# Kernel optimization log

Measured on AMD Instinct MI355X. Metric: run time of the kernel, lower is better.

## Reference

```python
import jax, jax.numpy as jnp
import numpy as np

OOV_INDEX = 1  # stand-in for params.OOV_INDEX
H = 1024
VOCAB = 50000
L = 2048


def setup_inputs() -> dict:
    key = jax.random.key(0)
    ks = jax.random.split(key, 10)
    s = 0.05
    inp = {
        "input_ids": jax.random.randint(ks[0], (L,), 0, VOCAB),
        "embedding": jax.random.normal(ks[1], (VOCAB, H), jnp.float32) * s,
        "fwd_W_ih": jax.random.normal(ks[2], (3 * H, H), jnp.float32) * s,
        "fwd_W_hh": jax.random.normal(ks[3], (3 * H, H), jnp.float32) * s,
        "fwd_b_ih": jax.random.normal(ks[4], (3 * H,), jnp.float32) * s,
        "fwd_b_hh": jax.random.normal(ks[5], (3 * H,), jnp.float32) * s,
        "rev_W_ih": jax.random.normal(ks[6], (3 * H, H), jnp.float32) * s,
        "rev_W_hh": jax.random.normal(ks[7], (3 * H, H), jnp.float32) * s,
        "rev_b_ih": jax.random.normal(ks[8], (3 * H,), jnp.float32) * s,
        "rev_b_hh": jax.random.normal(ks[9], (3 * H,), jnp.float32) * s,
    }
    return inp


def _gru_scan(x_seq, W_ih, W_hh, b_ih, b_hh):
    # x_seq: [L, H]. PyTorch GRU gate order: r, z, n.
    gx = x_seq @ W_ih.T + b_ih  # [L, 3H], input projections precomputed

    def step(h, gx_t):
        gh = h @ W_hh.T + b_hh
        gx_r, gx_z, gx_n = jnp.split(gx_t, 3)
        gh_r, gh_z, gh_n = jnp.split(gh, 3)
        r = jax.nn.sigmoid(gx_r + gh_r)
        z = jax.nn.sigmoid(gx_z + gh_z)
        n = jnp.tanh(gx_n + r * gh_n)
        h_new = (1.0 - z) * n + z * h
        return h_new, h_new

    h0 = jnp.zeros((x_seq.shape[1],), x_seq.dtype)
    h_last, outs = jax.lax.scan(step, h0, gx)
    return outs, h_last  # [L, H], [H]


def reference(input_ids, embedding, fwd_W_ih, fwd_W_hh, fwd_b_ih, fwd_b_hh,
              rev_W_ih, rev_W_hh, rev_b_ih, rev_b_hh):
    # Embedding lookup; OOV index -> zero vector (empty_vector in original)
    embeds = embedding[input_ids]  # [L, H]
    embeds = jnp.where((input_ids == OOV_INDEX)[:, None], 0.0, embeds)

    fwd_outputs, fwd_h = _gru_scan(embeds, fwd_W_ih, fwd_W_hh, fwd_b_ih, fwd_b_hh)
    rev_outs_rev, rev_h = _gru_scan(embeds[::-1], rev_W_ih, rev_W_hh, rev_b_ih, rev_b_hh)
    rev_outputs = rev_outs_rev[::-1]  # place back at original positions

    outputs = jnp.concatenate([fwd_outputs, rev_outputs], axis=1)  # [L, 2H]
    hidden = jnp.concatenate([fwd_h, rev_h])[None, None, :]        # [1, 1, 2H]
    projected_output = hidden
    return outputs, hidden, projected_output
```

## Files before the change

### kernel.cpp

```cpp
#include <hip/hip_runtime.h>
#include <math.h>

#define SEQL 2048
#define H 1024
#define G3 3072
#define SENT 1.0e30f

__device__ __forceinline__ float sigmoidf_(float x){ return 1.0f/(1.0f+expf(-x)); }

__device__ __forceinline__ float2 ld_cohere2(const float* p){
  float2 r;
  asm volatile("global_load_dwordx2 %0, %1, off sc0 sc1\n\t"
               "s_waitcnt vmcnt(0)"
               : "=&v"(r) : "v"(p) : "memory");
  return r;
}
__device__ __forceinline__ void st_cohere1(float* p, float v){
  asm volatile("global_store_dword %0, %1, off sc0 sc1"
               :: "v"(p), "v"(v) : "memory");
}

__global__ __launch_bounds__(256) void init_sent(float* p, int n4){
  int i = blockIdx.x*256 + threadIdx.x;
  if (i < n4) ((float4*)p)[i] = make_float4(SENT,SENT,SENT,SENT);
}

__global__ __launch_bounds__(256) void embed_kernel(const int* __restrict__ ids,
                                                    const float* __restrict__ emb,
                                                    float* __restrict__ out){
  int t = blockIdx.x;
  int id = ids[t];
  const float4* src = (const float4*)(emb + (size_t)id*H);
  float4* dst = (float4*)(out + (size_t)t*H);
  float4 v = (id == 1) ? make_float4(0.f,0.f,0.f,0.f) : src[threadIdx.x];
  dst[threadIdx.x] = v;
}

__global__ __launch_bounds__(256) void gemm_kernel(const float* __restrict__ A,
  const float* __restrict__ WF, const float* __restrict__ WR,
  const float* __restrict__ bF, const float* __restrict__ bR,
  float* __restrict__ gxF, float* __restrict__ gxR)
{
  __shared__ float As[16][68];
  __shared__ float Bs[16][68];
  const int tid = threadIdx.x;
  const int n0 = blockIdx.x * 64;
  const int m0 = blockIdx.y * 64;
  const int dir = (n0 >= G3);
  const float* B    = dir ? WR : WF;
  const float* bias = dir ? bR : bF;
  float* C          = dir ? gxR : gxF;
  const int j0 = dir ? (n0 - G3) : n0;

  const int lr = tid >> 2;
  const int lc = (tid & 3) * 4;
  const int tx = tid & 15;
  const int ty = tid >> 4;

  float acc[4][4] = {};

  for (int k0 = 0; k0 < H; k0 += 16){
    float4 av = *(const float4*)(A + (size_t)(m0+lr)*H + k0 + lc);
    float4 bv = *(const float4*)(B + (size_t)(j0+lr)*H + k0 + lc);
    As[lc+0][lr]=av.x; As[lc+1][lr]=av.y; As[lc+2][lr]=av.z; As[lc+3][lr]=av.w;
    Bs[lc+0][lr]=bv.x; Bs[lc+1][lr]=bv.y; Bs[lc+2][lr]=bv.z; Bs[lc+3][lr]=bv.w;
    __syncthreads();
    #pragma unroll
    for (int kk=0; kk<16; ++kk){
      float a0=As[kk][ty*4+0], a1=As[kk][ty*4+1], a2=As[kk][ty*4+2], a3=As[kk][ty*4+3];
      float b0=Bs[kk][tx*4+0], b1=Bs[kk][tx*4+1], b2=Bs[kk][tx*4+2], b3=Bs[kk][tx*4+3];
      acc[0][0]=fmaf(a0,b0,acc[0][0]); acc[0][1]=fmaf(a0,b1,acc[0][1]);
      acc[0][2]=fmaf(a0,b2,acc[0][2]); acc[0][3]=fmaf(a0,b3,acc[0][3]);
      acc[1][0]=fmaf(a1,b0,acc[1][0]); acc[1][1]=fmaf(a1,b1,acc[1][1]);
      acc[1][2]=fmaf(a1,b2,acc[1][2]); acc[1][3]=fmaf(a1,b3,acc[1][3]);
      acc[2][0]=fmaf(a2,b0,acc[2][0]); acc[2][1]=fmaf(a2,b1,acc[2][1]);
      acc[2][2]=fmaf(a2,b2,acc[2][2]); acc[2][3]=fmaf(a2,b3,acc[2][3]);
      acc[3][0]=fmaf(a3,b0,acc[3][0]); acc[3][1]=fmaf(a3,b1,acc[3][1]);
      acc[3][2]=fmaf(a3,b2,acc[3][2]); acc[3][3]=fmaf(a3,b3,acc[3][3]);
    }
    __syncthreads();
  }

  #pragma unroll
  for (int u=0; u<4; ++u){
    float4 o;
    o.x = acc[u][0] + bias[j0+tx*4+0];
    o.y = acc[u][1] + bias[j0+tx*4+1];
    o.z = acc[u][2] + bias[j0+tx*4+2];
    o.w = acc[u][3] + bias[j0+tx*4+3];
    *(float4*)(C + (size_t)(m0+ty*4+u)*G3 + j0 + tx*4) = o;
  }
}

__global__ __launch_bounds__(512, 1) void scan_kernel(
  const float* __restrict__ gxF, const float* __restrict__ gxR,
  const float* __restrict__ WhF, const float* __restrict__ WhR,
  const float* __restrict__ bhF, const float* __restrict__ bhR,
  float* hFbuf, float* hRbuf, float* __restrict__ out)
{
  const int wgid = blockIdx.x;
  const int dir  = wgid >> 7;
  const int d    = wgid & 127;
  const int i0   = d * 8;
  const int tid  = threadIdx.x;
  const int lane = tid & 63;
  const int wv   = tid >> 6;

  const float* gx  = dir ? gxR : gxF;
  const float* Whh = dir ? WhR : WhF;
  const float* bhh = dir ? bhR : bhF;
  float* hbuf      = dir ? hRbuf : hFbuf;

  const int ia = i0 + wv;
  const int rows[3] = { ia, H+ia, 2*H+ia };

  float w[3][16];
  float bias[3];
  #pragma unroll
  for (int rr=0; rr<3; ++rr){
    const float* wp = Whh + (size_t)rows[rr]*H + lane;
    #pragma unroll
    for (int m=0; m<16; ++m) w[rr][m] = wp[m*64];
    bias[rr] = bhh[rows[rr]];
  }
  #pragma unroll
  for (int rr=0; rr<3; ++rr){
    #pragma unroll
    for (int m=0; m<16; ++m) asm volatile("" : "+v"(w[rr][m]));
    asm volatile("" : "+v"(bias[rr]));
  }

  __shared__ float hs[H];

  for (int s=0; s<SEQL; ++s){
    const int t = dir ? (SEQL-1-s) : s;
    const float* gxt = gx + (size_t)t*G3;
    float g0 = gxt[ia], g1 = gxt[H+ia], g2 = gxt[2*H+ia];

    if (s == 0){
      hs[tid*2+0] = 0.0f; hs[tid*2+1] = 0.0f;
    } else {
      const float* src = hbuf + (size_t)(s-1)*H + tid*2;
      float2 v;
      do { v = ld_cohere2(src); }
      while (v.x==SENT || v.y==SENT);
      hs[tid*2+0]=v.x; hs[tid*2+1]=v.y;
    }
    __syncthreads();

    float hv[16];
    #pragma unroll
    for (int m=0; m<16; ++m) hv[m] = hs[lane + 64*m];

    float dots[3];
    #pragma unroll
    for (int rr=0; rr<3; ++rr){
      float acc = 0.f;
      #pragma unroll
      for (int m=0; m<16; ++m) acc = fmaf(w[rr][m], hv[m], acc);
      #pragma unroll
      for (int off=32; off>0; off>>=1) acc += __shfl_xor(acc, off);
      dots[rr] = acc + bias[rr];
    }

    const float hp = hs[ia];
    float r = sigmoidf_(g0 + dots[0]);
    float z = sigmoidf_(g1 + dots[1]);
    float n = tanhf    (g2 + r*dots[2]);
    float hn = (1.f - z)*n + z*hp;

    if (lane == 0){
      st_cohere1(hbuf + (size_t)s*H + ia, hn);
      out[(size_t)t*2048 + dir*H + ia] = hn;
      if (s == SEQL-1){
        const size_t base = (size_t)SEQL*2048;
        out[base + dir*H + ia]        = hn;
        out[base + 2048 + dir*H + ia] = hn;
      }
    }
    __syncthreads();
  }
}

extern "C" void kernel_launch(void* const* d_in, const int* in_sizes, int n_in,
                              void* d_out, int out_size, void* d_ws, size_t ws_size,
                              hipStream_t stream)
{
  const int*   ids  = (const int*)  d_in[0];
  const float* emb  = (const float*)d_in[1];
  const float* WihF = (const float*)d_in[2];
  const float* WhhF = (const float*)d_in[3];
  const float* bihF = (const float*)d_in[4];
  const float* bhhF = (const float*)d_in[5];
  const float* WihR = (const float*)d_in[6];
  const float* WhhR = (const float*)d_in[7];
  const float* bihR = (const float*)d_in[8];
  const float* bhhR = (const float*)d_in[9];
  float* out = (float*)d_out;
  float* ws  = (float*)d_ws;

  float* embeds = ws;
  float* gxF    = embeds + (size_t)SEQL*H;
  float* gxR    = gxF + (size_t)SEQL*G3;
  float* hF     = gxR + (size_t)SEQL*G3;
  float* hR     = hF + (size_t)SEQL*H;

  init_sent<<<4096, 256, 0, stream>>>(hF, 1048576);
  embed_kernel<<<SEQL, 256, 0, stream>>>(ids, emb, embeds);
  dim3 gg(96, 32);
  gemm_kernel<<<gg, 256, 0, stream>>>(embeds, WihF, WihR, bihF, bihR, gxF, gxR);
  scan_kernel<<<256, 512, 0, stream>>>(gxF, gxR, WhhF, WhhR, bhhF, bhhR, hF, hR, out);
}
```

Measured before the change: 6.236 ms.

## Double-buffer hidden state in LDS, drop trailing barrier, stash weights in AGPRs

The recurrent scan now double-buffers the shared hidden-state vector so the barrier at the end of each step can be removed, leaving one barrier per step. The polling load is widened to float4 across 256 threads, and the LDS reads use float4 with a matching permuted weight layout. Recurrent weights are held in accumulation registers and copied back to VGPRs every step, which frees VGPRs but adds 48 register moves per step. The goal is to shorten the serial per-step latency of the 2048-step recurrence.

```diff
diff --git a/kernel.cpp b/kernel.cpp
--- a/kernel.cpp
+++ b/kernel.cpp
@@ -8,9 +8,9 @@
 
 __device__ __forceinline__ float sigmoidf_(float x){ return 1.0f/(1.0f+expf(-x)); }
 
-__device__ __forceinline__ float2 ld_cohere2(const float* p){
-  float2 r;
-  asm volatile("global_load_dwordx2 %0, %1, off sc0 sc1\n\t"
+__device__ __forceinline__ float4 ld_cohere4(const float* p){
+  float4 r;
+  asm volatile("global_load_dwordx4 %0, %1, off sc0 sc1\n\t"
                "s_waitcnt vmcnt(0)"
                : "=&v"(r) : "v"(p) : "memory");
   return r;
@@ -114,56 +114,67 @@
   const int ia = i0 + wv;
   const int rows[3] = { ia, H+ia, 2*H+ia };
 
-  float w[3][16];
+  float wa[48];
   float bias[3];
   #pragma unroll
   for (int rr=0; rr<3; ++rr){
-    const float* wp = Whh + (size_t)rows[rr]*H + lane;
-    #pragma unroll
-    for (int m=0; m<16; ++m) w[rr][m] = wp[m*64];
     bias[rr] = bhh[rows[rr]];
-  }
-  #pragma unroll
-  for (int rr=0; rr<3; ++rr){
-    #pragma unroll
-    for (int m=0; m<16; ++m) asm volatile("" : "+v"(w[rr][m]));
-    asm volatile("" : "+v"(bias[rr]));
-  }
-
-  __shared__ float hs[H];
+    const float* wp = Whh + (size_t)rows[rr]*H;
+    #pragma unroll
+    for (int q=0; q<4; ++q){
+      float4 w4 = *(const float4*)(wp + q*256 + lane*4);
+      asm volatile("v_accvgpr_write_b32 %0, %1" : "=a"(wa[rr*16+q*4+0]) : "v"(w4.x));
+      asm volatile("v_accvgpr_write_b32 %0, %1" : "=a"(wa[rr*16+q*4+1]) : "v"(w4.y));
+      asm volatile("v_accvgpr_write_b32 %0, %1" : "=a"(wa[rr*16+q*4+2]) : "v"(w4.z));
+      asm volatile("v_accvgpr_write_b32 %0, %1" : "=a"(wa[rr*16+q*4+3]) : "v"(w4.w));
+    }
+  }
+
+  __shared__ float hs[2][H];
 
   for (int s=0; s<SEQL; ++s){
+    const int b = s & 1;
     const int t = dir ? (SEQL-1-s) : s;
     const float* gxt = gx + (size_t)t*G3;
     float g0 = gxt[ia], g1 = gxt[H+ia], g2 = gxt[2*H+ia];
-
-    if (s == 0){
-      hs[tid*2+0] = 0.0f; hs[tid*2+1] = 0.0f;
-    } else {
-      const float* src = hbuf + (size_t)(s-1)*H + tid*2;
-      float2 v;
-      do { v = ld_cohere2(src); }
-      while (v.x==SENT || v.y==SENT);
-      hs[tid*2+0]=v.x; hs[tid*2+1]=v.y;
+    float wr[48];
+    #pragma unroll
+    for (int i=0; i<48; ++i)
+      asm volatile("v_accvgpr_read_b32 %0, %1" : "=v"(wr[i]) : "a"(wa[i]));
+
+    if (tid < 256){
+      float4* dst = (float4*)&hs[b][tid*4];
+      if (s == 0){
+        *dst = make_float4(0.f,0.f,0.f,0.f);
+      } else {
+        const float* src = hbuf + (size_t)(s-1)*H + tid*4;
+        float4 v;
+        do { v = ld_cohere4(src); }
+        while (v.x==SENT || v.y==SENT || v.z==SENT || v.w==SENT);
+        *dst = v;
+      }
     }
     __syncthreads();
 
     float hv[16];
     #pragma unroll
-    for (int m=0; m<16; ++m) hv[m] = hs[lane + 64*m];
+    for (int q=0; q<4; ++q){
+      float4 hq = *(const float4*)&hs[b][q*256 + lane*4];
+      hv[q*4+0]=hq.x; hv[q*4+1]=hq.y; hv[q*4+2]=hq.z; hv[q*4+3]=hq.w;
+    }
 
     float dots[3];
     #pragma unroll
     for (int rr=0; rr<3; ++rr){
       float acc = 0.f;
       #pragma unroll
-      for (int m=0; m<16; ++m) acc = fmaf(w[rr][m], hv[m], acc);
+      for (int m=0; m<16; ++m) acc = fmaf(wr[rr*16+m], hv[m], acc);
       #pragma unroll
       for (int off=32; off>0; off>>=1) acc += __shfl_xor(acc, off);
       dots[rr] = acc + bias[rr];
     }
 
-    const float hp = hs[ia];
+    const float hp = hs[b][ia];
     float r = sigmoidf_(g0 + dots[0]);
     float z = sigmoidf_(g1 + dots[1]);
     float n = tanhf    (g2 + r*dots[2]);
@@ -178,7 +189,6 @@
         out[base + 2048 + dir*H + ia] = hn;
       }
     }
-    __syncthreads();
   }
 }
 
```

New measurement: 7.014 ms. +12.5%, slower.
